# Kernel optimization log

Measured on AMD Instinct MI355X. Metric: run time of the kernel, lower is better.

Reference implementation:

```python
import jax, jax.numpy as jnp
import numpy as np

B, N, L, ND = 512, 4096, 128, 1


def setup_inputs() -> dict:
    key = jax.random.key(0)
    ks = jax.random.split(key, 20)
    g = lambda k, shape, s=0.05: jax.random.normal(k, shape, dtype=jnp.float32) * s
    IN = 3 * L + ND  # MLP input: [mem, mem, delta_t, x]
    inp = {
        "x": jax.random.normal(ks[0], (B, N, ND), jnp.float32),
        "memory": jax.random.normal(ks[1], (N, L), jnp.float32),
        "delta_t": jax.random.normal(ks[2], (B, N, L), jnp.float32),
        "src_w1": g(ks[3], (L, IN)), "src_b1": g(ks[4], (L,)),
        "src_w2": g(ks[5], (L, L)), "src_b2": g(ks[6], (L,)),
        "tar_w1": g(ks[7], (L, IN)), "tar_b1": g(ks[8], (L,)),
        "tar_w2": g(ks[9], (L, L)), "tar_b2": g(ks[10], (L,)),
        "gru_wih": g(ks[11], (3 * L, L)), "gru_whh": g(ks[12], (3 * L, L)),
        "gru_bih": g(ks[13], (3 * L,)), "gru_bhh": g(ks[14], (3 * L,)),
        "source": jax.random.randint(ks[15], (B, 1), 0, N, dtype=jnp.int64),
        "target": jax.random.randint(ks[16], (B, 1), 0, N, dtype=jnp.int64),
    }
    return inp


def _mlp(h, w1, b1, w2, b2):
    return jax.nn.relu(h @ w1.T + b1) @ w2.T + b2


def _gru_cell(inp, h, wih, whh, bih, bhh):
    gi = inp @ wih.T + bih          # [n, 3L]
    gh = h @ whh.T + bhh            # [n, 3L]
    i_r, i_z, i_n = jnp.split(gi, 3, axis=-1)
    h_r, h_z, h_n = jnp.split(gh, 3, axis=-1)
    r = jax.nn.sigmoid(i_r + h_r)
    z = jax.nn.sigmoid(i_z + h_z)
    n = jnp.tanh(i_n + r * h_n)
    return (1.0 - z) * n + z * h


def reference(x, memory, delta_t, src_w1, src_b1, src_w2, src_b2,
              tar_w1, tar_b1, tar_w2, tar_b2,
              gru_wih, gru_whh, gru_bih, gru_bhh, source, target):
    b = x.shape[0]
    bi = jnp.arange(b)
    s = source[:, 0]
    t = target[:, 0]
    src_mem = memory[s]                 # [B, L]
    tar_mem = memory[t]                 # [B, L]
    src_x = x[bi, s, :]                 # [B, ND]
    tar_x = x[bi, t, :]
    src_dt = delta_t[bi, s, :]          # [B, L]
    tar_dt = delta_t[bi, t, :]
    src_in = jnp.concatenate([src_mem, tar_mem, src_dt, src_x], axis=-1)
    tar_in = jnp.concatenate([tar_mem, src_mem, tar_dt, tar_x], axis=-1)
    src_msg = _mlp(src_in, src_w1, src_b1, src_w2, src_b2)
    tar_msg = _mlp(tar_in, tar_w1, tar_b1, tar_w2, tar_b2)

    # unique + scatter_mean == segment-mean over node ids, touching only seen nodes
    ids = jnp.concatenate([s, t], axis=0)                       # [2B]
    msgs = jnp.concatenate([src_msg, tar_msg], axis=0)          # [2B, L]
    n_nodes = memory.shape[0]
    msg_sum = jax.ops.segment_sum(msgs, ids, num_segments=n_nodes)
    cnt = jax.ops.segment_sum(jnp.ones((ids.shape[0],), msgs.dtype), ids,
                              num_segments=n_nodes)
    agg = msg_sum / jnp.maximum(cnt, 1.0)[:, None]              # [N, L]
    new_mem = _gru_cell(agg, memory, gru_wih, gru_whh, gru_bih, gru_bhh)
    seen = (cnt > 0)[:, None]
    return jnp.where(seen, new_mem, memory)
```

## Files before the change

kernel.cpp:

```cpp
#include <hip/hip_runtime.h>
#include <math.h>

#define BB 512
#define NN 4096
#define LL 128
#define IN_DIM 385
#define NK8_1 49
#define NK8_2 16
#define EPB 2
#define GPB 4

#define OFF_MSG   0
#define OFF_CNT   (OFF_MSG + NN * LL)
#define OFF_COUNT (OFF_CNT + NN)
#define OFF_LIST  (OFF_COUNT + 4)
#define OFF_W1BS  529416
#define OFF_W1BT  (OFF_W1BS + NK8_1 * LL * 4)
#define OFF_W2BS  (OFF_W1BT + NK8_1 * LL * 4)
#define OFF_W2BT  (OFF_W2BS + NK8_2 * LL * 4)
#define OFF_WIHB  (OFF_W2BT + NK8_2 * LL * 4)
#define OFF_WHHB  (OFF_WIHB + 3 * NK8_2 * LL * 4)

__device__ inline unsigned short f2bf(float f) {
    unsigned u = __float_as_uint(f);
    return (unsigned short)((u + 0x7fffu + ((u >> 16) & 1u)) >> 16);
}
__device__ inline unsigned pack2(float lo, float hi) {
    return (unsigned)f2bf(lo) | ((unsigned)f2bf(hi) << 16);
}
struct f8 { float v[8]; };
__device__ inline f8 unpack8(uint4 u) {
    f8 r;
    r.v[0] = __uint_as_float(u.x << 16); r.v[1] = __uint_as_float(u.x & 0xffff0000u);
    r.v[2] = __uint_as_float(u.y << 16); r.v[3] = __uint_as_float(u.y & 0xffff0000u);
    r.v[4] = __uint_as_float(u.z << 16); r.v[5] = __uint_as_float(u.z & 0xffff0000u);
    r.v[6] = __uint_as_float(u.w << 16); r.v[7] = __uint_as_float(u.w & 0xffff0000u);
    return r;
}

__global__ __launch_bounds__(256) void prep_kernel(
    const float* __restrict__ sw1, const float* __restrict__ tw1,
    const float* __restrict__ sw2, const float* __restrict__ tw2,
    const float* __restrict__ wih, const float* __restrict__ whh,
    float* __restrict__ ws)
{
    const int i = blockIdx.x * 256 + threadIdx.x;
    const int stride = gridDim.x * 256;

    float4* msg4 = (float4*)(ws + OFF_MSG);
    const float4 z4 = make_float4(0.f, 0.f, 0.f, 0.f);
    for (int idx = i; idx < NN * LL / 4; idx += stride)
        msg4[idx] = z4;
    for (int idx = i; idx < NN; idx += stride)
        ws[OFF_CNT + idx] = 0.0f;
    if (i == 0)
        ((int*)ws)[OFF_COUNT] = 0;

    uint4* w1bs = (uint4*)(ws + OFF_W1BS);
    uint4* w1bt = (uint4*)(ws + OFF_W1BT);
    for (int idx = i; idx < NK8_1 * LL; idx += stride) {
        const int k8 = idx >> 7, j = idx & 127;
        const int k = k8 * 8;
        float a[8], b[8];
        #pragma unroll
        for (int c = 0; c < 8; ++c) {
            a[c] = (k + c < IN_DIM) ? sw1[j * IN_DIM + k + c] : 0.f;
            b[c] = (k + c < IN_DIM) ? tw1[j * IN_DIM + k + c] : 0.f;
        }
        w1bs[idx] = make_uint4(pack2(a[0], a[1]), pack2(a[2], a[3]),
                               pack2(a[4], a[5]), pack2(a[6], a[7]));
        w1bt[idx] = make_uint4(pack2(b[0], b[1]), pack2(b[2], b[3]),
                               pack2(b[4], b[5]), pack2(b[6], b[7]));
    }
    uint4* w2bs = (uint4*)(ws + OFF_W2BS);
    uint4* w2bt = (uint4*)(ws + OFF_W2BT);
    for (int idx = i; idx < NK8_2 * LL; idx += stride) {
        const int k8 = idx >> 7, j = idx & 127;
        const int k = k8 * 8;
        const float* pa = sw2 + j * LL + k;
        const float* pb = tw2 + j * LL + k;
        w2bs[idx] = make_uint4(pack2(pa[0], pa[1]), pack2(pa[2], pa[3]),
                               pack2(pa[4], pa[5]), pack2(pa[6], pa[7]));
        w2bt[idx] = make_uint4(pack2(pb[0], pb[1]), pack2(pb[2], pb[3]),
                               pack2(pb[4], pb[5]), pack2(pb[6], pb[7]));
    }
    uint4* wihb = (uint4*)(ws + OFF_WIHB);
    uint4* whhb = (uint4*)(ws + OFF_WHHB);
    for (int idx = i; idx < 3 * NK8_2 * LL; idx += stride) {
        const int j = idx & 127;
        const int gk = idx >> 7;
        const int gate = gk >> 4, k8 = gk & 15;
        const float* pa = wih + (gate * LL + j) * LL + k8 * 8;
        const float* pb = whh + (gate * LL + j) * LL + k8 * 8;
        wihb[idx] = make_uint4(pack2(pa[0], pa[1]), pack2(pa[2], pa[3]),
                               pack2(pa[4], pa[5]), pack2(pa[6], pa[7]));
        whhb[idx] = make_uint4(pack2(pb[0], pb[1]), pack2(pb[2], pb[3]),
                               pack2(pb[4], pb[5]), pack2(pb[6], pb[7]));
    }
}

#define BF8_STEP(WU, A0, A1, B0, B1) {                                  \
    const f8 W_ = unpack8(WU);                                          \
    a0 = fmaf(W_.v[0], (A0).x, a0); a1 = fmaf(W_.v[0], (B0).x, a1);     \
    a0 = fmaf(W_.v[1], (A0).y, a0); a1 = fmaf(W_.v[1], (B0).y, a1);     \
    a0 = fmaf(W_.v[2], (A0).z, a0); a1 = fmaf(W_.v[2], (B0).z, a1);     \
    a0 = fmaf(W_.v[3], (A0).w, a0); a1 = fmaf(W_.v[3], (B0).w, a1);     \
    a0 = fmaf(W_.v[4], (A1).x, a0); a1 = fmaf(W_.v[4], (B1).x, a1);     \
    a0 = fmaf(W_.v[5], (A1).y, a0); a1 = fmaf(W_.v[5], (B1).y, a1);     \
    a0 = fmaf(W_.v[6], (A1).z, a0); a1 = fmaf(W_.v[6], (B1).z, a1);     \
    a0 = fmaf(W_.v[7], (A1).w, a0); a1 = fmaf(W_.v[7], (B1).w, a1); }

__global__ __launch_bounds__(256) void edge_msg_kernel(
    const float* __restrict__ x,
    const float* __restrict__ memory,
    const float* __restrict__ delta_t,
    const float* __restrict__ sb1, const float* __restrict__ sb2,
    const float* __restrict__ tb1, const float* __restrict__ tb2,
    const int* __restrict__ source, const int* __restrict__ target,
    float* __restrict__ ws, float* __restrict__ out)
{
    const int tid = threadIdx.x;

    if (blockIdx.x >= 512) {
        const int cb = blockIdx.x - 512;
        float4* out4 = (float4*)out;
        const float4* mem4 = (const float4*)memory;
        for (int idx = cb * 256 + tid; idx < NN * LL / 4; idx += 32 * 256)
            out4[idx] = mem4[idx];
        return;
    }

    const int side  = blockIdx.x & 1;
    const int chunk = blockIdx.x >> 1;
    const int g     = tid >> 7;
    const int j     = tid & 127;

    const int eg0 = chunk * EPB, eg1 = eg0 + 1;
    const int s0 = source[eg0], t0 = target[eg0];
    const int s1 = source[eg1], t1 = target[eg1];
    const int node0  = side ? t0 : s0, other0 = side ? s0 : t0;
    const int node1  = side ? t1 : s1, other1 = side ? s1 : t1;

    __shared__ float h1s[EPB][LL];
    __shared__ float part1[2][EPB][LL];
    __shared__ float part2[2][EPB][LL];

    const uint4* w1b = (const uint4*)(ws + (side ? OFF_W1BT : OFF_W1BS));
    const uint4* w2b = (const uint4*)(ws + (side ? OFF_W2BT : OFF_W2BS));
    const float* b1  = side ? tb1 : sb1;
    const float* b2  = side ? tb2 : sb2;

    {
        float a0 = 0.f, a1 = 0.f;
        const float* nA = memory + (size_t)node0 * LL;
        const float* nB = memory + (size_t)node1 * LL;
        const float* oA = memory + (size_t)other0 * LL;
        const float* oB = memory + (size_t)other1 * LL;
        const float* dA = delta_t + ((size_t)eg0 * NN + node0) * LL;
        const float* dB = delta_t + ((size_t)eg1 * NN + node1) * LL;

        if (g == 0) {
            #pragma unroll 4
            for (int k8 = 0; k8 < 16; ++k8) {
                const uint4 wu = w1b[k8 * LL + j];
                const float4 A0 = *(const float4*)(nA + 8 * k8);
                const float4 A1 = *(const float4*)(nA + 8 * k8 + 4);
                const float4 B0 = *(const float4*)(nB + 8 * k8);
                const float4 B1 = *(const float4*)(nB + 8 * k8 + 4);
                BF8_STEP(wu, A0, A1, B0, B1)
            }
            #pragma unroll 4
            for (int k8 = 16; k8 < 24; ++k8) {
                const uint4 wu = w1b[k8 * LL + j];
                const float4 A0 = *(const float4*)(oA + 8 * k8 - 128);
                const float4 A1 = *(const float4*)(oA + 8 * k8 - 124);
                const float4 B0 = *(const float4*)(oB + 8 * k8 - 128);
                const float4 B1 = *(const float4*)(oB + 8 * k8 - 124);
                BF8_STEP(wu, A0, A1, B0, B1)
            }
        } else {
            #pragma unroll 4
            for (int k8 = 24; k8 < 32; ++k8) {
                const uint4 wu = w1b[k8 * LL + j];
                const float4 A0 = *(const float4*)(oA + 8 * k8 - 128);
                const float4 A1 = *(const float4*)(oA + 8 * k8 - 124);
                const float4 B0 = *(const float4*)(oB + 8 * k8 - 128);
                const float4 B1 = *(const float4*)(oB + 8 * k8 - 124);
                BF8_STEP(wu, A0, A1, B0, B1)
            }
            #pragma unroll 4
            for (int k8 = 32; k8 < 48; ++k8) {
                const uint4 wu = w1b[k8 * LL + j];
                const float4 A0 = *(const float4*)(dA + 8 * k8 - 256);
                const float4 A1 = *(const float4*)(dA + 8 * k8 - 252);
                const float4 B0 = *(const float4*)(dB + 8 * k8 - 256);
                const float4 B1 = *(const float4*)(dB + 8 * k8 - 252);
                BF8_STEP(wu, A0, A1, B0, B1)
            }
            {
                const uint4 wu = w1b[48 * LL + j];
                const float w0 = __uint_as_float(wu.x << 16);
                a0 = fmaf(w0, x[(size_t)eg0 * NN + node0], a0);
                a1 = fmaf(w0, x[(size_t)eg1 * NN + node1], a1);
            }
        }
        part1[g][0][j] = a0;
        part1[g][1][j] = a1;
    }
    __syncthreads();

    h1s[g][j] = fmaxf(part1[0][g][j] + part1[1][g][j] + b1[j], 0.0f);
    __syncthreads();

    {
        const int k80 = g * 8, k81 = k80 + 8;
        float a0 = 0.f, a1 = 0.f;
        #pragma unroll 4
        for (int k8 = k80; k8 < k81; ++k8) {
            const uint4 wu = w2b[k8 * LL + j];
            const float4 A0 = *(const float4*)&h1s[0][8 * k8];
            const float4 A1 = *(const float4*)&h1s[0][8 * k8 + 4];
            const float4 B0 = *(const float4*)&h1s[1][8 * k8];
            const float4 B1 = *(const float4*)&h1s[1][8 * k8 + 4];
            BF8_STEP(wu, A0, A1, B0, B1)
        }
        part2[g][0][j] = a0;
        part2[g][1][j] = a1;
    }
    __syncthreads();

    {
        const int node = g ? node1 : node0;
        const float m = part2[0][g][j] + part2[1][g][j] + b2[j];
        atomicAdd(ws + OFF_MSG + (size_t)node * LL + j, m);
    }
    if (tid < EPB) {
        const int node = tid ? node1 : node0;
        const float old = atomicAdd(ws + OFF_CNT + node, 1.0f);
        if (old == 0.0f) {
            const int pos = atomicAdd((int*)ws + OFF_COUNT, 1);
            ((int*)ws)[OFF_LIST + pos] = node;
        }
    }
}

__global__ __launch_bounds__(256) void gru_kernel(
    const float* __restrict__ memory,
    const float* __restrict__ bih, const float* __restrict__ bhh,
    const float* __restrict__ ws, float* __restrict__ out)
{
    const int tid = threadIdx.x;
    const int g = tid >> 7, j = tid & 127;
    const int scount = ((const int*)ws)[OFF_COUNT];
    const int base = blockIdx.x * GPB;
    if (base >= scount) return;
    const int nact = min(GPB, scount - base);

    __shared__ float gates[6][GPB][LL];
    __shared__ int   nodes_sh[GPB];

    int nd[GPB];
    #pragma unroll
    for (int s = 0; s < GPB; ++s)
        nd[s] = (base + s < scount) ? ((const int*)ws)[OFF_LIST + base + s]
                                    : ((const int*)ws)[OFF_LIST + base];
    if (tid < GPB) nodes_sh[tid] = nd[tid];

    const float* op[GPB];
    float rc[GPB] = {1.f, 1.f, 1.f, 1.f};
    #pragma unroll
    for (int s = 0; s < GPB; ++s) {
        if (g == 0) {
            op[s] = ws + OFF_MSG + (size_t)nd[s] * LL;
            rc[s] = 1.0f / ws[OFF_CNT + nd[s]];
        } else {
            op[s] = memory + (size_t)nd[s] * LL;
        }
    }

    const uint4* wpb = (const uint4*)(ws + (g ? OFF_WHHB : OFF_WIHB));
    float a0[GPB] = {}, a1[GPB] = {}, a2[GPB] = {};
    #pragma unroll 2
    for (int k8 = 0; k8 < NK8_2; ++k8) {
        const f8 w0 = unpack8(wpb[(0 * NK8_2 + k8) * LL + j]);
        const f8 w1 = unpack8(wpb[(1 * NK8_2 + k8) * LL + j]);
        const f8 w2 = unpack8(wpb[(2 * NK8_2 + k8) * LL + j]);
        #pragma unroll
        for (int s = 0; s < GPB; ++s) {
            const float4 v0 = *(const float4*)(op[s] + 8 * k8);
            const float4 v1 = *(const float4*)(op[s] + 8 * k8 + 4);
            const float v[8] = {v0.x, v0.y, v0.z, v0.w, v1.x, v1.y, v1.z, v1.w};
            #pragma unroll
            for (int c = 0; c < 8; ++c) {
                a0[s] = fmaf(w0.v[c], v[c], a0[s]);
                a1[s] = fmaf(w1.v[c], v[c], a1[s]);
                a2[s] = fmaf(w2.v[c], v[c], a2[s]);
            }
        }
    }
    #pragma unroll
    for (int s = 0; s < GPB; ++s) {
        gates[g * 3 + 0][s][j] = a0[s] * rc[s];
        gates[g * 3 + 1][s][j] = a1[s] * rc[s];
        gates[g * 3 + 2][s][j] = a2[s] * rc[s];
    }
    __syncthreads();

    const int total = nact * LL;
    for (int o = tid; o < total; o += 256) {
        const int s = o >> 7, jj = o & 127;
        const int node = nodes_sh[s];
        const float ir = gates[0][s][jj] + bih[jj];
        const float iz = gates[1][s][jj] + bih[LL + jj];
        const float inn = gates[2][s][jj] + bih[2 * LL + jj];
        const float hr = gates[3][s][jj] + bhh[jj];
        const float hz = gates[4][s][jj] + bhh[LL + jj];
        const float hn = gates[5][s][jj] + bhh[2 * LL + jj];
        const float r = 1.0f / (1.0f + __expf(-(ir + hr)));
        const float z = 1.0f / (1.0f + __expf(-(iz + hz)));
        const float n = tanhf(inn + r * hn);
        const float h = memory[(size_t)node * LL + jj];
        out[(size_t)node * LL + jj] = (1.0f - z) * n + z * h;
    }
}

extern "C" void kernel_launch(void* const* d_in, const int* in_sizes, int n_in,
                              void* d_out, int out_size, void* d_ws, size_t ws_size,
                              hipStream_t stream) {
    const float* x        = (const float*)d_in[0];
    const float* memory   = (const float*)d_in[1];
    const float* delta_t  = (const float*)d_in[2];
    const float* src_w1   = (const float*)d_in[3];
    const float* src_b1   = (const float*)d_in[4];
    const float* src_w2   = (const float*)d_in[5];
    const float* src_b2   = (const float*)d_in[6];
    const float* tar_w1   = (const float*)d_in[7];
    const float* tar_b1   = (const float*)d_in[8];
    const float* tar_w2   = (const float*)d_in[9];
    const float* tar_b2   = (const float*)d_in[10];
    const float* gru_wih  = (const float*)d_in[11];
    const float* gru_whh  = (const float*)d_in[12];
    const float* gru_bih  = (const float*)d_in[13];
    const float* gru_bhh  = (const float*)d_in[14];
    const int*   source   = (const int*)d_in[15];
    const int*   target   = (const int*)d_in[16];

    float* out = (float*)d_out;
    float* ws  = (float*)d_ws;

    prep_kernel<<<512, 256, 0, stream>>>(
        src_w1, tar_w1, src_w2, tar_w2, gru_wih, gru_whh, ws);

    edge_msg_kernel<<<544, 256, 0, stream>>>(
        x, memory, delta_t, src_b1, src_b2, tar_b1, tar_b2,
        source, target, ws, out);

    gru_kernel<<<1024 / GPB, 256, 0, stream>>>(
        memory, gru_bih, gru_bhh, ws, out);
}
```

Measured before the change: 34.96 us.

## Replace atomic scatter-sum with per-node linked lists of edge messages

Instead of zeroing a 2 MB per-node message buffer and atomically adding messages into it, each edge message is written to its own slot and linked into a per-node list via atomicExch on a head array. The GRU kernel walks each node's list to compute the mean, stages the aggregate and memory rows in shared memory, and reuses the staged memory row for the final blend. This removes the large zeroing pass and the float atomics, at the cost of serial pointer chasing in the GRU kernel. The prep grid is also halved.

```diff
diff --git a/kernel.cpp b/kernel.cpp
--- a/kernel.cpp
+++ b/kernel.cpp
@@ -8,13 +8,15 @@
 #define NK8_1 49
 #define NK8_2 16
 #define EPB 2
+#define TASKS 1024
 #define GPB 4
 
-#define OFF_MSG   0
-#define OFF_CNT   (OFF_MSG + NN * LL)
-#define OFF_COUNT (OFF_CNT + NN)
+#define OFF_MSGS  0
+#define OFF_HEAD  (OFF_MSGS + TASKS * LL)
+#define OFF_NEXT  (OFF_HEAD + NN)
+#define OFF_COUNT (OFF_NEXT + TASKS)
 #define OFF_LIST  (OFF_COUNT + 4)
-#define OFF_W1BS  529416
+#define OFF_W1BS  (OFF_LIST + 1024)
 #define OFF_W1BT  (OFF_W1BS + NK8_1 * LL * 4)
 #define OFF_W2BS  (OFF_W1BT + NK8_1 * LL * 4)
 #define OFF_W2BT  (OFF_W2BS + NK8_2 * LL * 4)
@@ -47,12 +49,9 @@
     const int i = blockIdx.x * 256 + threadIdx.x;
     const int stride = gridDim.x * 256;
 
-    float4* msg4 = (float4*)(ws + OFF_MSG);
-    const float4 z4 = make_float4(0.f, 0.f, 0.f, 0.f);
-    for (int idx = i; idx < NN * LL / 4; idx += stride)
-        msg4[idx] = z4;
+    int* heads = (int*)ws + OFF_HEAD;
     for (int idx = i; idx < NN; idx += stride)
-        ws[OFF_CNT + idx] = 0.0f;
+        heads[idx] = -1;
     if (i == 0)
         ((int*)ws)[OFF_COUNT] = 0;
 
@@ -230,14 +229,16 @@
     __syncthreads();
 
     {
-        const int node = g ? node1 : node0;
+        const int task = side * BB + (g ? eg1 : eg0);
         const float m = part2[0][g][j] + part2[1][g][j] + b2[j];
-        atomicAdd(ws + OFF_MSG + (size_t)node * LL + j, m);
+        ws[OFF_MSGS + (size_t)task * LL + j] = m;
     }
     if (tid < EPB) {
         const int node = tid ? node1 : node0;
-        const float old = atomicAdd(ws + OFF_CNT + node, 1.0f);
-        if (old == 0.0f) {
+        const int task = side * BB + (tid ? eg1 : eg0);
+        const int old = atomicExch((int*)ws + OFF_HEAD + node, task);
+        ((int*)ws)[OFF_NEXT + task] = old;
+        if (old == -1) {
             const int pos = atomicAdd((int*)ws + OFF_COUNT, 1);
             ((int*)ws)[OFF_LIST + pos] = node;
         }
@@ -256,8 +257,12 @@
     if (base >= scount) return;
     const int nact = min(GPB, scount - base);
 
+    __shared__ float ah[2 * GPB][LL];
     __shared__ float gates[6][GPB][LL];
     __shared__ int   nodes_sh[GPB];
+
+    const int* heads = (const int*)ws + OFF_HEAD;
+    const int* nexts = (const int*)ws + OFF_NEXT;
 
     int nd[GPB];
     #pragma unroll
@@ -266,17 +271,23 @@
                                     : ((const int*)ws)[OFF_LIST + base];
     if (tid < GPB) nodes_sh[tid] = nd[tid];
 
-    const float* op[GPB];
-    float rc[GPB] = {1.f, 1.f, 1.f, 1.f};
-    #pragma unroll
-    for (int s = 0; s < GPB; ++s) {
-        if (g == 0) {
-            op[s] = ws + OFF_MSG + (size_t)nd[s] * LL;
-            rc[s] = 1.0f / ws[OFF_CNT + nd[s]];
-        } else {
-            op[s] = memory + (size_t)nd[s] * LL;
-        }
-    }
+    if (g == 0) {
+        #pragma unroll
+        for (int s = 0; s < GPB; ++s) {
+            float acc = 0.0f;
+            int c = 0;
+            for (int t = heads[nd[s]]; t != -1; t = nexts[t]) {
+                acc += ws[OFF_MSGS + (size_t)t * LL + j];
+                ++c;
+            }
+            ah[s][j] = acc / (float)c;
+        }
+    } else {
+        #pragma unroll
+        for (int s = 0; s < GPB; ++s)
+            ah[GPB + s][j] = memory[(size_t)nd[s] * LL + j];
+    }
+    __syncthreads();
 
     const uint4* wpb = (const uint4*)(ws + (g ? OFF_WHHB : OFF_WIHB));
     float a0[GPB] = {}, a1[GPB] = {}, a2[GPB] = {};
@@ -287,8 +298,8 @@
         const f8 w2 = unpack8(wpb[(2 * NK8_2 + k8) * LL + j]);
         #pragma unroll
         for (int s = 0; s < GPB; ++s) {
-            const float4 v0 = *(const float4*)(op[s] + 8 * k8);
-            const float4 v1 = *(const float4*)(op[s] + 8 * k8 + 4);
+            const float4 v0 = *(const float4*)&ah[g * GPB + s][8 * k8];
+            const float4 v1 = *(const float4*)&ah[g * GPB + s][8 * k8 + 4];
             const float v[8] = {v0.x, v0.y, v0.z, v0.w, v1.x, v1.y, v1.z, v1.w};
             #pragma unroll
             for (int c = 0; c < 8; ++c) {
@@ -300,9 +311,9 @@
     }
     #pragma unroll
     for (int s = 0; s < GPB; ++s) {
-        gates[g * 3 + 0][s][j] = a0[s] * rc[s];
-        gates[g * 3 + 1][s][j] = a1[s] * rc[s];
-        gates[g * 3 + 2][s][j] = a2[s] * rc[s];
+        gates[g * 3 + 0][s][j] = a0[s];
+        gates[g * 3 + 1][s][j] = a1[s];
+        gates[g * 3 + 2][s][j] = a2[s];
     }
     __syncthreads();
 
@@ -319,7 +330,7 @@
         const float r = 1.0f / (1.0f + __expf(-(ir + hr)));
         const float z = 1.0f / (1.0f + __expf(-(iz + hz)));
         const float n = tanhf(inn + r * hn);
-        const float h = memory[(size_t)node * LL + jj];
+        const float h = ah[GPB + s][jj];
         out[(size_t)node * LL + jj] = (1.0f - z) * n + z * h;
     }
 }
@@ -348,7 +359,7 @@
     float* out = (float*)d_out;
     float* ws  = (float*)d_ws;
 
-    prep_kernel<<<512, 256, 0, stream>>>(
+    prep_kernel<<<256, 256, 0, stream>>>(
         src_w1, tar_w1, src_w2, tar_w2, gru_wih, gru_whh, ws);
 
     edge_msg_kernel<<<544, 256, 0, stream>>>(
```

New measurement: 32.51 us. -7.0%, faster.
